# Kernel tuning notes

Hardware: AMD Instinct MI355X
Metric: run time of the kernel (lower is better)

## Reference

```python
import jax, jax.numpy as jnp
import numpy as np

DIM = 8
N = 8388608


def _d8_quantize(x):
    """D8 lattice quantization of rows of x [N, 8].

    f = round(x); g = f with the coordinate of largest |x - f| nudged by +-1
    (toward x). Use g where sum(g) is even, else f (equivalent to the usual
    'use f if sum(f) even else g' rule, faithfully matching the torch code).
    """
    f = jnp.round(x)                                  # round-half-to-even, like torch
    d = x - f                                         # [N, 8]
    k = jnp.argmax(jnp.abs(d), axis=1)                # [N] coord with max |delta|
    dk = jnp.take_along_axis(d, k[:, None], axis=1)[:, 0]
    fix = jnp.where(dk < 0, -1.0, 1.0).astype(x.dtype)  # torch: fix=1, set -1 if delta<0
    g = f + jax.nn.one_hot(k, DIM, dtype=x.dtype) * fix[:, None]
    g_even = jnp.mod(jnp.sum(g, axis=1), 2.0) == 0.0  # [N]
    return jnp.where(g_even[:, None], g, f)


def setup_inputs() -> dict:
    key = jax.random.key(0)
    x = jax.random.normal(key, (N, DIM), dtype=jnp.float32)
    return {"x": x}


def reference(x):
    # E8 = D8 union (D8 + 1/2): quantize against both cosets, keep nearer point.
    y1 = _d8_quantize(x)
    y2 = _d8_quantize(x - 0.5) + 0.5
    s1 = jnp.linalg.norm(x - y1, axis=1)
    s2 = jnp.linalg.norm(x - y2, axis=1)
    # torch.argmin picks index 0 on ties -> choose y2 only when strictly smaller
    return jnp.where((s2 < s1)[:, None], y2, y1)
```

## Files before the change

### kernel.cpp

```cpp
#include <hip/hip_runtime.h>
#include <math.h>


__device__ __forceinline__ void d8_quant(const float x[8], float out[8]) {
#pragma clang fp contract(off)
    float f[8], d[8];
#pragma unroll
    for (int j = 0; j < 8; ++j) {
        f[j] = rintf(x[j]);
        d[j] = x[j] - f[j];
    }
    int k = 0;
    float best = fabsf(d[0]);
    float dk = d[0];
#pragma unroll
    for (int j = 1; j < 8; ++j) {
        float a = fabsf(d[j]);
        bool gt = a > best;
        best = gt ? a : best;
        dk   = gt ? d[j] : dk;
        k    = gt ? j : k;
    }
    float fix = (dk < 0.0f) ? -1.0f : 1.0f;
    float sumf = 0.0f;
#pragma unroll
    for (int j = 0; j < 8; ++j) sumf += f[j];
    int si = (int)sumf;
    float add = (si & 1) ? fix : 0.0f;
#pragma unroll
    for (int j = 0; j < 8; ++j) out[j] = f[j] + ((j == k) ? add : 0.0f);
}

__global__ __launch_bounds__(256) void e8_quant_kernel(
    const float4* __restrict__ in, float4* __restrict__ out, int nrows)
{
#pragma clang fp contract(off)
    int i = blockIdx.x * blockDim.x + threadIdx.x;
    if (i >= nrows) return;

    float4 a = in[2 * i];
    float4 b = in[2 * i + 1];
    float x[8] = {a.x, a.y, a.z, a.w, b.x, b.y, b.z, b.w};

    float y1[8], y2[8], t[8];
    d8_quant(x, y1);
#pragma unroll
    for (int j = 0; j < 8; ++j) t[j] = x[j] - 0.5f;
    d8_quant(t, y2);
#pragma unroll
    for (int j = 0; j < 8; ++j) y2[j] += 0.5f;

    float s1 = 0.0f, s2 = 0.0f;
#pragma unroll
    for (int j = 0; j < 8; ++j) { float e = x[j] - y1[j]; s1 += e * e; }
#pragma unroll
    for (int j = 0; j < 8; ++j) { float e = x[j] - y2[j]; s2 += e * e; }
    bool take2 = sqrtf(s2) < sqrtf(s1);

#pragma unroll
    for (int j = 0; j < 8; ++j) x[j] = take2 ? y2[j] : y1[j];

    out[2 * i]     = make_float4(x[0], x[1], x[2], x[3]);
    out[2 * i + 1] = make_float4(x[4], x[5], x[6], x[7]);
}

extern "C" void kernel_launch(void* const* d_in, const int* in_sizes, int n_in,
                              void* d_out, int out_size, void* d_ws, size_t ws_size,
                              hipStream_t stream) {
    const float* x = (const float*)d_in[0];
    float* o = (float*)d_out;
    int nrows = in_sizes[0] / 8;
    const int block = 256;
    const int grid = (nrows + block - 1) / block;
    e8_quant_kernel<<<grid, block, 0, stream>>>(
        (const float4*)x, (float4*)o, nrows);
}
```

Baseline: 424.7 us.

## Split each E8 row across two lanes with shuffle-based reductions

Each 8-wide row is now processed by two adjacent threads, each holding one float4. The argmax, coordinate sum and squared-error reductions are combined across the lane pair with xor shuffles. This doubles the thread count and gives each thread a single contiguous float4 load and store, so adjacent lanes touch adjacent 16-byte chunks for more coalesced memory access and fewer registers per thread. In exchange it adds cross-lane shuffle traffic, and the tie-breaking and summation order have to be reproduced exactly across the two halves.

```diff
diff --git a/kernel.cpp b/kernel.cpp
--- a/kernel.cpp
+++ b/kernel.cpp
@@ -2,76 +2,80 @@
 #include <math.h>
 
 
-__device__ __forceinline__ void d8_quant(const float x[8], float out[8]) {
-#pragma clang fp contract(off)
-    float f[8], d[8];
-#pragma unroll
-    for (int j = 0; j < 8; ++j) {
-        f[j] = rintf(x[j]);
-        d[j] = x[j] - f[j];
-    }
-    int k = 0;
-    float best = fabsf(d[0]);
-    float dk = d[0];
-#pragma unroll
-    for (int j = 1; j < 8; ++j) {
-        float a = fabsf(d[j]);
-        bool gt = a > best;
-        best = gt ? a : best;
-        dk   = gt ? d[j] : dk;
-        k    = gt ? j : k;
-    }
-    float fix = (dk < 0.0f) ? -1.0f : 1.0f;
-    float sumf = 0.0f;
-#pragma unroll
-    for (int j = 0; j < 8; ++j) sumf += f[j];
-    int si = (int)sumf;
-    float add = (si & 1) ? fix : 0.0f;
-#pragma unroll
-    for (int j = 0; j < 8; ++j) out[j] = f[j] + ((j == k) ? add : 0.0f);
-}
+__device__ __forceinline__ float sx1(float v) { return __shfl_xor(v, 1, 64); }
 
-__global__ __launch_bounds__(256) void e8_quant_kernel(
-    const float4* __restrict__ in, float4* __restrict__ out, int nrows)
+__global__ __launch_bounds__(256) void e8_quant_pair(
+    const float4* __restrict__ in, float4* __restrict__ out, int n4)
 {
 #pragma clang fp contract(off)
-    int i = blockIdx.x * blockDim.x + threadIdx.x;
-    if (i >= nrows) return;
+    int t = blockIdx.x * blockDim.x + threadIdx.x;
+    if (t >= n4) return;
+    const bool hi = (t & 1) != 0;
 
-    float4 a = in[2 * i];
-    float4 b = in[2 * i + 1];
-    float x[8] = {a.x, a.y, a.z, a.w, b.x, b.y, b.z, b.w};
+    float4 v = in[t];
+    float x[4] = {v.x, v.y, v.z, v.w};
 
-    float y1[8], y2[8], t[8];
-    d8_quant(x, y1);
+    float y[2][4];
 #pragma unroll
-    for (int j = 0; j < 8; ++j) t[j] = x[j] - 0.5f;
-    d8_quant(t, y2);
+    for (int c = 0; c < 2; ++c) {
+        const float h = c ? 0.5f : 0.0f;
+        float f[4], d[4];
 #pragma unroll
-    for (int j = 0; j < 8; ++j) y2[j] += 0.5f;
+        for (int j = 0; j < 4; ++j) {
+            float xc = x[j] - h;
+            f[j] = rintf(xc);
+            d[j] = xc - f[j];
+        }
+        float best = fabsf(d[0]); float dk = d[0]; int k = 0;
+#pragma unroll
+        for (int j = 1; j < 4; ++j) {
+            float a = fabsf(d[j]);
+            bool gt = a > best;
+            best = gt ? a : best; dk = gt ? d[j] : dk; k = gt ? j : k;
+        }
+        float ls = ((f[0] + f[1]) + f[2]) + f[3];
+        float obest = sx1(best);
+        float osum  = sx1(ls);
+        bool win = hi ? (best > obest) : (best >= obest);
+        float tot = ls + osum;
+        int par = ((int)tot) & 1;
+        float fix = (dk < 0.0f) ? -1.0f : 1.0f;
+        float add = (win && par) ? fix : 0.0f;
+#pragma unroll
+        for (int j = 0; j < 4; ++j)
+            y[c][j] = (f[j] + ((j == k) ? add : 0.0f)) + h;
+    }
 
-    float s1 = 0.0f, s2 = 0.0f;
+    float s[2];
 #pragma unroll
-    for (int j = 0; j < 8; ++j) { float e = x[j] - y1[j]; s1 += e * e; }
+    for (int c = 0; c < 2; ++c) {
+        float eq[4];
 #pragma unroll
-    for (int j = 0; j < 8; ++j) { float e = x[j] - y2[j]; s2 += e * e; }
-    bool take2 = sqrtf(s2) < sqrtf(s1);
+        for (int j = 0; j < 4; ++j) { float e = x[j] - y[c][j]; eq[j] = e * e; }
+        float pl = (((0.0f + eq[0]) + eq[1]) + eq[2]) + eq[3];
+        float q = sx1(pl);
+        float th = (((q + eq[0]) + eq[1]) + eq[2]) + eq[3];
+        float r = sx1(th);
+        s[c] = hi ? th : r;
+    }
 
-#pragma unroll
-    for (int j = 0; j < 8; ++j) x[j] = take2 ? y2[j] : y1[j];
+    bool take2 = sqrtf(s[1]) < sqrtf(s[0]);
 
-    out[2 * i]     = make_float4(x[0], x[1], x[2], x[3]);
-    out[2 * i + 1] = make_float4(x[4], x[5], x[6], x[7]);
+    float4 o;
+    o.x = take2 ? y[1][0] : y[0][0];
+    o.y = take2 ? y[1][1] : y[0][1];
+    o.z = take2 ? y[1][2] : y[0][2];
+    o.w = take2 ? y[1][3] : y[0][3];
+    out[t] = o;
 }
 
 extern "C" void kernel_launch(void* const* d_in, const int* in_sizes, int n_in,
                               void* d_out, int out_size, void* d_ws, size_t ws_size,
                               hipStream_t stream) {
-    const float* x = (const float*)d_in[0];
-    float* o = (float*)d_out;
-    int nrows = in_sizes[0] / 8;
+    const float4* x = (const float4*)d_in[0];
+    float4* o = (float4*)d_out;
+    int n4 = in_sizes[0] / 4;
     const int block = 256;
-    const int grid = (nrows + block - 1) / block;
-    e8_quant_kernel<<<grid, block, 0, stream>>>(
-        (const float4*)x, (float4*)o, nrows);
+    const int grid = (n4 + block - 1) / block;
+    e8_quant_pair<<<grid, block, 0, stream>>>(x, o, n4);
 }
```

Result: faster. 411.3 us (-3.2%).
